# Kernel tuning notes

Measured on AMD Instinct MI355X. Metric: run time of the kernel, lower is better.

Reference implementation:

```python
import jax, jax.numpy as jnp
import numpy as np

L, B, E, H = 1024, 8, 1024, 16
HD = E // H
SCALE = HD ** -0.5
EPS = 1e-5


def setup_inputs() -> dict:
    key = jax.random.key(0)
    ks = jax.random.split(key, 6)
    s = E ** -0.5
    return {
        "x": jax.random.normal(ks[0], (L, B, E), dtype=jnp.float32),
        "attn_mask": jnp.zeros((L, L), dtype=jnp.float32),
        "Wq": jax.random.normal(ks[1], (E, E), dtype=jnp.float32) * s,
        "bq": jnp.zeros((E,), dtype=jnp.float32),
        "Wk": jax.random.normal(ks[2], (E, E), dtype=jnp.float32) * s,
        "bk": jnp.zeros((E,), dtype=jnp.float32),
        "Wv": jax.random.normal(ks[3], (E, E), dtype=jnp.float32) * s,
        "bv": jnp.zeros((E,), dtype=jnp.float32),
        "Wo": jax.random.normal(ks[4], (E, E), dtype=jnp.float32) * s,
        "bo": jnp.zeros((E,), dtype=jnp.float32),
        "gamma": jnp.ones((E,), dtype=jnp.float32),
        "beta": jnp.zeros((E,), dtype=jnp.float32),
    }


def _layernorm(x, gamma, beta):
    mu = jnp.mean(x, axis=-1, keepdims=True)
    var = jnp.mean(jnp.square(x - mu), axis=-1, keepdims=True)
    return (x - mu) * jax.lax.rsqrt(var + EPS) * gamma + beta


def reference(x, attn_mask, Wq, bq, Wk, bk, Wv, bv, Wo, bo, gamma, beta):
    # x: (L, B, E); pre-LN residual attention block (dropout=0, eval)
    ln_x = _layernorm(x, gamma, beta)
    # torch Linear: y = x @ W.T + b
    q = (ln_x @ Wq.T + bq) * SCALE
    k = ln_x @ Wk.T + bk
    v = ln_x @ Wv.T + bv
    # (L, B, E) -> (B, H, L, hd)
    def split_heads(t):
        return t.reshape(L, B, H, HD).transpose(1, 2, 0, 3)
    q, k, v = split_heads(q), split_heads(k), split_heads(v)
    # full attention matrix, as in the original non-fused bmm path
    attn = jnp.einsum('bhqd,bhkd->bhqk', q, k) + attn_mask[None, None]
    attn = jax.nn.softmax(attn, axis=-1)
    out = jnp.einsum('bhqk,bhkd->bhqd', attn, v)  # (B, H, L, hd)
    out = out.transpose(2, 0, 1, 3).reshape(L, B, E)
    out = out @ Wo.T + bo
    return x + out
```

## Files before the change

kernel.cpp:

```cpp
#include <hip/hip_runtime.h>

#define LL 1024
#define BB 8
#define EE 1024
#define HH 16
#define HD 64
#define MROWS (LL*BB)

typedef __attribute__((ext_vector_type(8))) short short8v;
typedef __attribute__((ext_vector_type(4))) float f32x4;
typedef __attribute__((ext_vector_type(16))) float f32x16;

#define LOG2E 1.44269504088896f

__device__ __forceinline__ unsigned short tobf(float f) {
    union { float f; unsigned u; } un; un.f = f;
    unsigned u = un.u;
    u += 0x7fffu + ((u >> 16) & 1u);
    return (unsigned short)(u >> 16);
}

__device__ __forceinline__ float max3f(float a, float b, float c) {
    return fmaxf(fmaxf(a, b), c);
}

__device__ __forceinline__ void load_lds16(const unsigned short* g, unsigned short* l) {
    __builtin_amdgcn_global_load_lds((const __attribute__((address_space(1))) unsigned int*)g,
                                     (__attribute__((address_space(3))) unsigned int*)l,
                                     16, 0, 0);
}

__global__ __launch_bounds__(256) void convw4_kernel(const float* __restrict__ w0,
                                                     const float* __restrict__ w1,
                                                     const float* __restrict__ w2,
                                                     const float* __restrict__ w3,
                                                     unsigned short* __restrict__ o0,
                                                     unsigned short* __restrict__ o1,
                                                     unsigned short* __restrict__ o2,
                                                     unsigned short* __restrict__ o3) {
    const float* w; unsigned short* o;
    switch (blockIdx.y) {
        case 0:  w = w0; o = o0; break;
        case 1:  w = w1; o = o1; break;
        case 2:  w = w2; o = o2; break;
        default: w = w3; o = o3; break;
    }
    int i = (blockIdx.x * 256 + threadIdx.x) * 4;
    float4 v = *(const float4*)&w[i];
    ushort4 r;
    r.x = tobf(v.x); r.y = tobf(v.y); r.z = tobf(v.z); r.w = tobf(v.w);
    *(ushort4*)&o[i] = r;
}

__global__ __launch_bounds__(256) void maskprep_kernel(const float* __restrict__ m,
                                                       unsigned* __restrict__ o) {
    __shared__ float t_sh[64][65];
    const int q0 = blockIdx.x * 64, k0 = blockIdx.y * 64;
    const int tid = threadIdx.x;
    {
        const int r = tid >> 2, c0 = (tid & 3) * 16;
        #pragma unroll
        for (int i = 0; i < 4; ++i) {
            float4 v = *(const float4*)&m[(size_t)(q0 + r) * LL + k0 + c0 + i*4];
            t_sh[r][c0+i*4+0] = v.x; t_sh[r][c0+i*4+1] = v.y;
            t_sh[r][c0+i*4+2] = v.z; t_sh[r][c0+i*4+3] = v.w;
        }
    }
    __syncthreads();
    const int k2l = tid >> 3, qi = (tid & 7) * 8;
    unsigned pk[8];
    #pragma unroll
    for (int j = 0; j < 8; ++j) {
        const unsigned lo = tobf(t_sh[qi+j][2*k2l]   * LOG2E);
        const unsigned hb = tobf(t_sh[qi+j][2*k2l+1] * LOG2E);
        pk[j] = lo | (hb << 16);
    }
    unsigned* orow = &o[(size_t)(k0/2 + k2l) * LL + q0 + qi];
    *(uint4*)&orow[0] = make_uint4(pk[0], pk[1], pk[2], pk[3]);
    *(uint4*)&orow[4] = make_uint4(pk[4], pk[5], pk[6], pk[7]);
}

__global__ __launch_bounds__(256) void ln_kernel(const float* __restrict__ x,
                                                 const float* __restrict__ gamma,
                                                 const float* __restrict__ beta,
                                                 unsigned short* __restrict__ out) {
    const int row = blockIdx.x;
    const int tid = threadIdx.x;
    const float4 v = *(const float4*)&x[(size_t)row * EE + tid * 4];
    float s = v.x + v.y + v.z + v.w;
    float q = v.x*v.x + v.y*v.y + v.z*v.z + v.w*v.w;
    #pragma unroll
    for (int off = 1; off < 64; off <<= 1) {
        s += __shfl_xor(s, off);
        q += __shfl_xor(q, off);
    }
    __shared__ float ss[4], sq[4];
    const int wv = tid >> 6;
    if ((tid & 63) == 0) { ss[wv] = s; sq[wv] = q; }
    __syncthreads();
    s = ss[0] + ss[1] + ss[2] + ss[3];
    q = sq[0] + sq[1] + sq[2] + sq[3];
    const float mu = s * (1.0f / EE);
    const float var = q * (1.0f / EE) - mu * mu;
    const float rs = rsqrtf(var + 1e-5f);
    ushort4 o;
    o.x = tobf((v.x - mu) * rs * gamma[tid*4+0] + beta[tid*4+0]);
    o.y = tobf((v.y - mu) * rs * gamma[tid*4+1] + beta[tid*4+1]);
    o.z = tobf((v.z - mu) * rs * gamma[tid*4+2] + beta[tid*4+2]);
    o.w = tobf((v.w - mu) * rs * gamma[tid*4+3] + beta[tid*4+3]);
    *(ushort4*)&out[(size_t)row * EE + tid * 4] = o;
}

#define GEMM128_BODY(A_, W_)                                                              \
    __shared__ unsigned short a_sh[2][128*32];                                            \
    __shared__ unsigned short b_sh[2][128*32];                                            \
    const int tid = threadIdx.x, lane = tid & 63, wave = tid >> 6;                        \
    const int bm = blockIdx.y * 128, bn = blockIdx.x * 128;                               \
    const int wr = (wave >> 1) * 64, wc = (wave & 1) * 64;                                \
    const int l16 = lane & 15, lk8 = (lane >> 4) * 8;                                     \
    const int grow = lane >> 2, gcol = (lane & 3) * 8;                                    \
    f32x4 acc[4][4] = {};                                                                 \
    _Pragma("unroll")                                                                     \
    for (int i = 0; i < 2; ++i) {                                                         \
        const int ch = wave * 2 + i;                                                      \
        load_lds16(&A_[(size_t)(bm + ch*16 + grow)*EE + gcol], &a_sh[0][ch*512]);         \
        load_lds16(&W_[(size_t)(bn + ch*16 + grow)*EE + gcol], &b_sh[0][ch*512]);         \
    }                                                                                     \
    __syncthreads();                                                                      \
    for (int k0 = 0; k0 < EE; k0 += 32) {                                                 \
        const int cur = (k0 >> 5) & 1;                                                    \
        if (k0 + 32 < EE) {                                                               \
            _Pragma("unroll")                                                             \
            for (int i = 0; i < 2; ++i) {                                                 \
                const int ch = wave * 2 + i;                                              \
                load_lds16(&A_[(size_t)(bm + ch*16 + grow)*EE + k0 + 32 + gcol], &a_sh[cur^1][ch*512]); \
                load_lds16(&W_[(size_t)(bn + ch*16 + grow)*EE + k0 + 32 + gcol], &b_sh[cur^1][ch*512]); \
            }                                                                             \
        }                                                                                 \
        short8v af[4], bf[4];                                                             \
        _Pragma("unroll")                                                                 \
        for (int mi = 0; mi < 4; ++mi) af[mi] = *(const short8v*)&a_sh[cur][(wr + mi*16 + l16)*32 + lk8]; \
        _Pragma("unroll")                                                                 \
        for (int ni = 0; ni < 4; ++ni) bf[ni] = *(const short8v*)&b_sh[cur][(wc + ni*16 + l16)*32 + lk8]; \
        _Pragma("unroll")                                                                 \
        for (int mi = 0; mi < 4; ++mi)                                                    \
            _Pragma("unroll")                                                             \
            for (int ni = 0; ni < 4; ++ni)                                                \
                acc[mi][ni] = __builtin_amdgcn_mfma_f32_16x16x32_bf16(af[mi], bf[ni], acc[mi][ni], 0, 0, 0); \
        __syncthreads();                                                                  \
    }

__global__ __launch_bounds__(256) void gemm_qkv(const unsigned short* __restrict__ A,
                                                const unsigned short* __restrict__ W,
                                                const float* __restrict__ bq,
                                                const float* __restrict__ bk,
                                                const float* __restrict__ bv,
                                                unsigned short* __restrict__ qo,
                                                unsigned short* __restrict__ ko,
                                                unsigned short* __restrict__ vo) {
    GEMM128_BODY(A, W)
    const int seg = blockIdx.x >> 3;
    const float* bias = seg == 0 ? bq : (seg == 1 ? bk : bv);
    #pragma unroll
    for (int mi = 0; mi < 4; ++mi) {
        #pragma unroll
        for (int ni = 0; ni < 4; ++ni) {
            #pragma unroll
            for (int r = 0; r < 4; ++r) {
                const int m  = bm + wr + mi*16 + (lane >> 4)*4 + r;
                const int nn = (bn & 1023) + wc + ni*16 + l16;
                const float v = acc[mi][ni][r] + bias[nn];
                const int l = m >> 3, b = m & 7, h = nn >> 6, d = nn & 63;
                if (seg == 0)      qo[((size_t)(b*HH + h) * LL + l) * HD + d] = tobf(v * (0.125f * LOG2E));
                else if (seg == 1) ko[((size_t)(b*HH + h) * LL + l) * HD + d] = tobf(v);
                else               vo[((size_t)(b*HH + h) * HD + d) * LL + l] = tobf(v);
            }
        }
    }
}

__global__ __launch_bounds__(256) void gemm_o(const unsigned short* __restrict__ A,
                                              const unsigned short* __restrict__ W,
                                              const float* __restrict__ bias,
                                              const float* __restrict__ xres,
                                              float* __restrict__ outf) {
    GEMM128_BODY(A, W)
    #pragma unroll
    for (int mi = 0; mi < 4; ++mi) {
        #pragma unroll
        for (int ni = 0; ni < 4; ++ni) {
            #pragma unroll
            for (int r = 0; r < 4; ++r) {
                const int m = bm + wr + mi*16 + (lane >> 4)*4 + r;
                const int n = bn + wc + ni*16 + l16;
                outf[(size_t)m * EE + n] = acc[mi][ni][r] + bias[n] + xres[(size_t)m * EE + n];
            }
        }
    }
}

__global__ __launch_bounds__(256) void attn_kernel(const unsigned short* __restrict__ qarr,
                                                   const unsigned short* __restrict__ karr,
                                                   const unsigned short* __restrict__ vtarr,
                                                   const unsigned* __restrict__ maskT2,
                                                   unsigned short* __restrict__ attn_out) {
    __shared__ __attribute__((aligned(16))) unsigned short k_sh[2][64*64];
    __shared__ __attribute__((aligned(16))) unsigned short v_sh[2][64*64];
    const int tid = threadIdx.x, lane = tid & 63, wave = tid >> 6;
    const int l32 = lane & 31, hi = lane >> 5;
    const int bh = blockIdx.y;
    const int qtok = blockIdx.x * 128 + wave * 32 + l32;
    const unsigned short* qb = qarr  + (size_t)bh * LL * HD;
    const unsigned short* kb = karr  + (size_t)bh * LL * HD;
    const unsigned short* vb = vtarr + (size_t)bh * HD * LL;

    short8v qf[4];
    #pragma unroll
    for (int dc = 0; dc < 4; ++dc)
        qf[dc] = *(const short8v*)&qb[(size_t)qtok * HD + dc*16 + hi*8];

    f32x16 acc[2] = {};
    float mrun = -1e30f, srun = 0.f;

    auto stage = [&](int buf, int kv) {
        #pragma unroll
        for (int i = 0; i < 2; ++i) {
            const int r = wave*16 + i*8 + (lane >> 3);
            const int c = ((lane & 7) ^ (r & 7)) * 8;
            load_lds16(&kb[(size_t)(kv + r) * HD + c], &k_sh[buf][(wave*16 + i*8) * 64]);
            load_lds16(&vb[(size_t)r * LL + kv + c],   &v_sh[buf][(wave*16 + i*8) * 64]);
        }
    };

    auto finish = [&](f32x16& s, const unsigned* mu, int sub, int buf) {
        #pragma unroll
        for (int j = 0; j < 8; ++j) {
            s[2*j]   += __uint_as_float(mu[j] << 16);
            s[2*j+1] += __uint_as_float(mu[j] & 0xffff0000u);
        }
        const float a0 = max3f(s[0],  s[1],  s[2]);
        const float a1 = max3f(s[3],  s[4],  s[5]);
        const float a2 = max3f(s[6],  s[7],  s[8]);
        const float a3 = max3f(s[9],  s[10], s[11]);
        const float a4 = max3f(s[12], s[13], s[14]);
        float pm = fmaxf(max3f(a0, a1, a2), max3f(a3, a4, s[15]));
        pm = fmaxf(pm, __shfl_xor(pm, 32));
        if (__any(pm - mrun > 8.0f)) {
            const float mn = fmaxf(mrun, pm);
            const float al = exp2f(mrun - mn);
            #pragma unroll
            for (int i = 0; i < 16; ++i) { acc[0][i] *= al; acc[1][i] *= al; }
            srun *= al;
            mrun = mn;
        }
        float p[16];
        #pragma unroll
        for (int i = 0; i < 16; ++i) p[i] = exp2f(s[i] - mrun);
        const float t0 = p[0]+p[1],   t1 = p[2]+p[3],   t2 = p[4]+p[5],   t3 = p[6]+p[7];
        const float t4 = p[8]+p[9],   t5 = p[10]+p[11], t6 = p[12]+p[13], t7 = p[14]+p[15];
        const float u0 = t0+t1, u1 = t2+t3, u2 = t4+t5, u3 = t6+t7;
        float rs = (u0+u1) + (u2+u3);
        rs += __shfl_xor(rs, 32);
        srun += rs;
        unsigned w[8];
        #pragma unroll
        for (int j = 0; j < 8; ++j)
            asm("v_cvt_pk_bf16_f32 %0, %1, %2" : "=v"(w[j]) : "v"(p[2*j]), "v"(p[2*j+1]));
        asm volatile("v_permlane32_swap_b32 %0, %1" : "+v"(w[0]), "+v"(w[2]));
        asm volatile("v_permlane32_swap_b32 %0, %1" : "+v"(w[1]), "+v"(w[3]));
        asm volatile("v_permlane32_swap_b32 %0, %1" : "+v"(w[4]), "+v"(w[6]));
        asm volatile("v_permlane32_swap_b32 %0, %1" : "+v"(w[5]), "+v"(w[7]));
        union { uint4 u; short8v s8; } pb0, pb1;
        pb0.u = make_uint4(w[0], w[1], w[2], w[3]);
        pb1.u = make_uint4(w[4], w[5], w[6], w[7]);
        __builtin_amdgcn_s_setprio(1);
        #pragma unroll
        for (int dt = 0; dt < 2; ++dt) {
            const int row = dt*32 + l32;
            const short8v vf0 = *(const short8v*)((const char*)&v_sh[buf][0]
                                  + (size_t)row*128 + ((((sub*2+0)*2 + hi) ^ (l32 & 7)) * 16));
            const short8v vf1 = *(const short8v*)((const char*)&v_sh[buf][0]
                                  + (size_t)row*128 + ((((sub*2+1)*2 + hi) ^ (l32 & 7)) * 16));
            acc[dt] = __builtin_amdgcn_mfma_f32_32x32x16_bf16(vf0, pb0.s8, acc[dt], 0, 0, 0);
            acc[dt] = __builtin_amdgcn_mfma_f32_32x32x16_bf16(vf1, pb1.s8, acc[dt], 0, 0, 0);
        }
        __builtin_amdgcn_s_setprio(0);
    };

    const unsigned* mt2base = maskT2 + qtok;
    stage(0, 0);
    const int NT = LL / 64;
    for (int t = 0; t < NT; ++t) {
        const int buf = t & 1;
        __syncthreads();
        if (t < NT - 1) stage(buf ^ 1, (t + 1) * 64);

        const unsigned* mt2 = mt2base + (size_t)t * 32 * LL;
        unsigned mu0[8], mu1[8];
        #pragma unroll
        for (int j = 0; j < 8; ++j)
            mu0[j] = mt2[(size_t)((j & 1) + 4*(j >> 1) + 2*hi) * LL];
        f32x16 s0 = {}, s1 = {};
        __builtin_amdgcn_s_setprio(1);
        #pragma unroll
        for (int dc = 0; dc < 4; ++dc) {
            const short8v kf = *(const short8v*)((const char*)&k_sh[buf][0]
                                 + (size_t)(l32)*128 + (((dc*2 + hi) ^ (l32 & 7)) * 16));
            s0 = __builtin_amdgcn_mfma_f32_32x32x16_bf16(kf, qf[dc], s0, 0, 0, 0);
        }
        #pragma unroll
        for (int dc = 0; dc < 4; ++dc) {
            const short8v kf = *(const short8v*)((const char*)&k_sh[buf][0]
                                 + (size_t)(32 + l32)*128 + (((dc*2 + hi) ^ (l32 & 7)) * 16));
            s1 = __builtin_amdgcn_mfma_f32_32x32x16_bf16(kf, qf[dc], s1, 0, 0, 0);
        }
        __builtin_amdgcn_s_setprio(0);
        #pragma unroll
        for (int j = 0; j < 8; ++j)
            mu1[j] = mt2[(size_t)(16 + (j & 1) + 4*(j >> 1) + 2*hi) * LL];
        finish(s0, mu0, 0, buf);
        finish(s1, mu1, 1, buf);
    }
    const float inv = 1.0f / srun;
    const int b = bh >> 4, h = bh & 15;
    unsigned short* orow = attn_out + ((size_t)qtok * BB + b) * EE + h * HD;
    #pragma unroll
    for (int dt = 0; dt < 2; ++dt) {
        #pragma unroll
        for (int g = 0; g < 4; ++g) {
            const float a0 = acc[dt][4*g+0]*inv, a1 = acc[dt][4*g+1]*inv;
            const float a2 = acc[dt][4*g+2]*inv, a3 = acc[dt][4*g+3]*inv;
            unsigned lo, hw;
            asm("v_cvt_pk_bf16_f32 %0, %1, %2" : "=v"(lo) : "v"(a0), "v"(a1));
            asm("v_cvt_pk_bf16_f32 %0, %1, %2" : "=v"(hw) : "v"(a2), "v"(a3));
            *(uint2*)&orow[dt*32 + g*8 + hi*4] = make_uint2(lo, hw);
        }
    }
}

extern "C" void kernel_launch(void* const* d_in, const int* in_sizes, int n_in,
                              void* d_out, int out_size, void* d_ws, size_t ws_size,
                              hipStream_t stream) {
    (void)in_sizes; (void)n_in; (void)out_size; (void)ws_size;
    const float* x     = (const float*)d_in[0];
    const float* mask  = (const float*)d_in[1];
    const float* Wq    = (const float*)d_in[2];
    const float* bq    = (const float*)d_in[3];
    const float* Wk    = (const float*)d_in[4];
    const float* bk    = (const float*)d_in[5];
    const float* Wv    = (const float*)d_in[6];
    const float* bv    = (const float*)d_in[7];
    const float* Wo    = (const float*)d_in[8];
    const float* bo    = (const float*)d_in[9];
    const float* gamma = (const float*)d_in[10];
    const float* beta  = (const float*)d_in[11];
    float* out = (float*)d_out;

    unsigned short* ws   = (unsigned short*)d_ws;
    unsigned short* ln   = ws;
    unsigned short* wqkv = ln   + (size_t)MROWS * EE;
    unsigned short* wob  = wqkv + (size_t)3 * EE * EE;
    unsigned short* qb   = wob  + (size_t)EE * EE;
    unsigned short* kbp  = qb   + (size_t)BB * HH * LL * HD;
    unsigned short* vtb  = kbp  + (size_t)BB * HH * LL * HD;
    unsigned short* attnb = ln;
    unsigned* maskT2 = (unsigned*)wqkv;

    convw4_kernel<<<dim3(1024, 4), 256, 0, stream>>>(
        Wq, Wk, Wv, Wo,
        wqkv, wqkv + (size_t)EE * EE, wqkv + (size_t)2 * EE * EE, wob);
    ln_kernel<<<MROWS, 256, 0, stream>>>(x, gamma, beta, ln);

    gemm_qkv<<<dim3(24, 64), 256, 0, stream>>>(ln, wqkv, bq, bk, bv, qb, kbp, vtb);

    maskprep_kernel<<<dim3(16, 16), 256, 0, stream>>>(mask, maskT2);

    attn_kernel<<<dim3(LL / 128, BB * HH), 256, 0, stream>>>(qb, kbp, vtb, maskT2, attnb);

    gemm_o<<<dim3(8, 64), 256, 0, stream>>>(attnb, wob, bo, x, out);
}
```

Measured before the change: 238.2 us.

## Triple-buffer GEMM and attention LDS staging with swizzled tiles and mask prefetch

Moves the QKV/output GEMM body and the attention kernel from double to triple LDS buffering. A single barrier per iteration, gated by explicit vmcnt waits, replaces the previous pair of full syncthreads, so global-to-LDS loads run two stages ahead. The GEMM tiles also get an XOR swizzle on their LDS layout to cut bank conflicts on fragment reads. The attention kernel now prefetches the next tile's mask values one iteration early. The cost is more LDS per block, which may lower occupancy, and the hand-counted vmcnt values are fragile if the load order changes.

Measured after the change: 239.8 us. About the same (+0.7%).

```diff
diff --git a/kernel.cpp b/kernel.cpp
--- a/kernel.cpp
+++ b/kernel.cpp
@@ -112,42 +112,59 @@
 }
 
 #define GEMM128_BODY(A_, W_)                                                              \
-    __shared__ unsigned short a_sh[2][128*32];                                            \
-    __shared__ unsigned short b_sh[2][128*32];                                            \
+    __shared__ unsigned short a_sh[3][128*32];                                            \
+    __shared__ unsigned short b_sh[3][128*32];                                            \
     const int tid = threadIdx.x, lane = tid & 63, wave = tid >> 6;                        \
     const int bm = blockIdx.y * 128, bn = blockIdx.x * 128;                               \
     const int wr = (wave >> 1) * 64, wc = (wave & 1) * 64;                                \
-    const int l16 = lane & 15, lk8 = (lane >> 4) * 8;                                     \
-    const int grow = lane >> 2, gcol = (lane & 3) * 8;                                    \
+    const int l16 = lane & 15, q4 = lane >> 4;                                            \
+    const int grow = lane >> 2;                                                           \
+    const int gswz = (((lane & 3) ^ (grow & 3)) * 8);                                     \
+    const int rslot = (q4 ^ (l16 & 3)) * 16;                       \
     f32x4 acc[4][4] = {};                                                                 \
+                                                           \
     _Pragma("unroll")                                                                     \
     for (int i = 0; i < 2; ++i) {                                                         \
         const int ch = wave * 2 + i;                                                      \
-        load_lds16(&A_[(size_t)(bm + ch*16 + grow)*EE + gcol], &a_sh[0][ch*512]);         \
-        load_lds16(&W_[(size_t)(bn + ch*16 + grow)*EE + gcol], &b_sh[0][ch*512]);         \
+        load_lds16(&A_[(size_t)(bm + ch*16 + grow)*EE + gswz], &a_sh[0][ch*512]);         \
+        load_lds16(&W_[(size_t)(bn + ch*16 + grow)*EE + gswz], &b_sh[0][ch*512]);         \
     }                                                                                     \
-    __syncthreads();                                                                      \
-    for (int k0 = 0; k0 < EE; k0 += 32) {                                                 \
-        const int cur = (k0 >> 5) & 1;                                                    \
-        if (k0 + 32 < EE) {                                                               \
+    _Pragma("unroll")                                                                     \
+    for (int i = 0; i < 2; ++i) {                                                         \
+        const int ch = wave * 2 + i;                                                      \
+        load_lds16(&A_[(size_t)(bm + ch*16 + grow)*EE + 32 + gswz], &a_sh[1][ch*512]);    \
+        load_lds16(&W_[(size_t)(bn + ch*16 + grow)*EE + 32 + gswz], &b_sh[1][ch*512]);    \
+    }                                                                                     \
+    int buf = 0, sb = 2;                                                                  \
+    for (int it = 0; it < 32; ++it) {                                                     \
+        if (it < 31) asm volatile("s_waitcnt vmcnt(4)" ::: "memory");                     \
+        else         asm volatile("s_waitcnt vmcnt(0)" ::: "memory");                     \
+        __builtin_amdgcn_s_barrier();                                                     \
+        if (it < 30) {                                                                    \
+            const int kn = (it + 2) * 32;                                                 \
             _Pragma("unroll")                                                             \
             for (int i = 0; i < 2; ++i) {                                                 \
                 const int ch = wave * 2 + i;                                              \
-                load_lds16(&A_[(size_t)(bm + ch*16 + grow)*EE + k0 + 32 + gcol], &a_sh[cur^1][ch*512]); \
-                load_lds16(&W_[(size_t)(bn + ch*16 + grow)*EE + k0 + 32 + gcol], &b_sh[cur^1][ch*512]); \
+                load_lds16(&A_[(size_t)(bm + ch*16 + grow)*EE + kn + gswz], &a_sh[sb][ch*512]); \
+                load_lds16(&W_[(size_t)(bn + ch*16 + grow)*EE + kn + gswz], &b_sh[sb][ch*512]); \
             }                                                                             \
         }                                                                                 \
         short8v af[4], bf[4];                                                             \
         _Pragma("unroll")                                                                 \
-        for (int mi = 0; mi < 4; ++mi) af[mi] = *(const short8v*)&a_sh[cur][(wr + mi*16 + l16)*32 + lk8]; \
+        for (int mi = 0; mi < 4; ++mi)                                                    \
+            af[mi] = *(const short8v*)((const char*)&a_sh[buf][0] + (size_t)(wr + mi*16 + l16)*64 + rslot); \
         _Pragma("unroll")                                                                 \
-        for (int ni = 0; ni < 4; ++ni) bf[ni] = *(const short8v*)&b_sh[cur][(wc + ni*16 + l16)*32 + lk8]; \
+        for (int ni = 0; ni < 4; ++ni)                                                    \
+            bf[ni] = *(const short8v*)((const char*)&b_sh[buf][0] + (size_t)(wc + ni*16 + l16)*64 + rslot); \
+        __builtin_amdgcn_s_setprio(1);                                                    \
         _Pragma("unroll")                                                                 \
         for (int mi = 0; mi < 4; ++mi)                                                    \
             _Pragma("unroll")                                                             \
             for (int ni = 0; ni < 4; ++ni)                                                \
                 acc[mi][ni] = __builtin_amdgcn_mfma_f32_16x16x32_bf16(af[mi], bf[ni], acc[mi][ni], 0, 0, 0); \
-        __syncthreads();                                                                  \
+        __builtin_amdgcn_s_setprio(0);                                                    \
+        buf = (buf == 2) ? 0 : buf + 1;                                                   \
+        sb  = (sb  == 2) ? 0 : sb  + 1;                                                   \
     }
 
 __global__ __launch_bounds__(256) void gemm_qkv(const unsigned short* __restrict__ A,
@@ -204,8 +221,8 @@
                                                    const unsigned short* __restrict__ vtarr,
                                                    const unsigned* __restrict__ maskT2,
                                                    unsigned short* __restrict__ attn_out) {
-    __shared__ __attribute__((aligned(16))) unsigned short k_sh[2][64*64];
-    __shared__ __attribute__((aligned(16))) unsigned short v_sh[2][64*64];
+    __shared__ __attribute__((aligned(16))) unsigned short k_sh[3][64*64];
+    __shared__ __attribute__((aligned(16))) unsigned short v_sh[3][64*64];
     const int tid = threadIdx.x, lane = tid & 63, wave = tid >> 6;
     const int l32 = lane & 31, hi = lane >> 5;
     const int bh = blockIdx.y;
@@ -222,17 +239,17 @@
     f32x16 acc[2] = {};
     float mrun = -1e30f, srun = 0.f;
 
-    auto stage = [&](int buf, int kv) {
+    auto stage = [&](int bufi, int kv) {
         #pragma unroll
         for (int i = 0; i < 2; ++i) {
             const int r = wave*16 + i*8 + (lane >> 3);
             const int c = ((lane & 7) ^ (r & 7)) * 8;
-            load_lds16(&kb[(size_t)(kv + r) * HD + c], &k_sh[buf][(wave*16 + i*8) * 64]);
-            load_lds16(&vb[(size_t)r * LL + kv + c],   &v_sh[buf][(wave*16 + i*8) * 64]);
+            load_lds16(&kb[(size_t)(kv + r) * HD + c], &k_sh[bufi][(wave*16 + i*8) * 64]);
+            load_lds16(&vb[(size_t)r * LL + kv + c],   &v_sh[bufi][(wave*16 + i*8) * 64]);
         }
     };
 
-    auto finish = [&](f32x16& s, const unsigned* mu, int sub, int buf) {
+    auto finish = [&](f32x16& s, const unsigned* mu, int sub, int bufi) {
         #pragma unroll
         for (int j = 0; j < 8; ++j) {
             s[2*j]   += __uint_as_float(mu[j] << 16);
@@ -277,9 +294,9 @@
         #pragma unroll
         for (int dt = 0; dt < 2; ++dt) {
             const int row = dt*32 + l32;
-            const short8v vf0 = *(const short8v*)((const char*)&v_sh[buf][0]
+            const short8v vf0 = *(const short8v*)((const char*)&v_sh[bufi][0]
                                   + (size_t)row*128 + ((((sub*2+0)*2 + hi) ^ (l32 & 7)) * 16));
-            const short8v vf1 = *(const short8v*)((const char*)&v_sh[buf][0]
+            const short8v vf1 = *(const short8v*)((const char*)&v_sh[bufi][0]
                                   + (size_t)row*128 + ((((sub*2+1)*2 + hi) ^ (l32 & 7)) * 16));
             acc[dt] = __builtin_amdgcn_mfma_f32_32x32x16_bf16(vf0, pb0.s8, acc[dt], 0, 0, 0);
             acc[dt] = __builtin_amdgcn_mfma_f32_32x32x16_bf16(vf1, pb1.s8, acc[dt], 0, 0, 0);
@@ -289,17 +306,30 @@
 
     const unsigned* mt2base = maskT2 + qtok;
     stage(0, 0);
+    unsigned mcur[16], mnxt[16];
+    #pragma unroll
+    for (int j = 0; j < 8; ++j) {
+        mcur[j]     = mt2base[(size_t)((j & 1) + 4*(j >> 1) + 2*hi) * LL];
+        mcur[8 + j] = mt2base[(size_t)(16 + (j & 1) + 4*(j >> 1) + 2*hi) * LL];
+    }
+    stage(1, 64);
+
     const int NT = LL / 64;
+    int buf = 0, sb = 2;
     for (int t = 0; t < NT; ++t) {
-        const int buf = t & 1;
-        __syncthreads();
-        if (t < NT - 1) stage(buf ^ 1, (t + 1) * 64);
-
-        const unsigned* mt2 = mt2base + (size_t)t * 32 * LL;
-        unsigned mu0[8], mu1[8];
-        #pragma unroll
-        for (int j = 0; j < 8; ++j)
-            mu0[j] = mt2[(size_t)((j & 1) + 4*(j >> 1) + 2*hi) * LL];
+        if (t < NT - 1) asm volatile("s_waitcnt vmcnt(4)" ::: "memory");
+        else            asm volatile("s_waitcnt vmcnt(0)" ::: "memory");
+        __builtin_amdgcn_s_barrier();
+        if (t < NT - 1) {
+            const unsigned* mt2n = mt2base + (size_t)(t + 1) * 32 * LL;
+            #pragma unroll
+            for (int j = 0; j < 8; ++j) {
+                mnxt[j]     = mt2n[(size_t)((j & 1) + 4*(j >> 1) + 2*hi) * LL];
+                mnxt[8 + j] = mt2n[(size_t)(16 + (j & 1) + 4*(j >> 1) + 2*hi) * LL];
+            }
+        }
+        if (t + 2 < NT) stage(sb, (t + 2) * 64);
+
         f32x16 s0 = {}, s1 = {};
         __builtin_amdgcn_s_setprio(1);
         #pragma unroll
@@ -315,11 +345,12 @@
             s1 = __builtin_amdgcn_mfma_f32_32x32x16_bf16(kf, qf[dc], s1, 0, 0, 0);
         }
         __builtin_amdgcn_s_setprio(0);
-        #pragma unroll
-        for (int j = 0; j < 8; ++j)
-            mu1[j] = mt2[(size_t)(16 + (j & 1) + 4*(j >> 1) + 2*hi) * LL];
-        finish(s0, mu0, 0, buf);
-        finish(s1, mu1, 1, buf);
+        finish(s0, &mcur[0], 0, buf);
+        finish(s1, &mcur[8], 1, buf);
+        #pragma unroll
+        for (int j = 0; j < 16; ++j) mcur[j] = mnxt[j];
+        buf = (buf == 2) ? 0 : buf + 1;
+        sb  = (sb  == 2) ? 0 : sb  + 1;
     }
     const float inv = 1.0f / srun;
     const int b = bh >> 4, h = bh & 15;
```
